# Kernel optimization log

Measured on AMD Instinct MI355X. Metric: run time of the kernel, lower is better.

The kernel has to match this reference:

```python
import jax, jax.numpy as jnp
import numpy as np


def setup_inputs() -> dict:
    key = jax.random.key(0)
    ks = jax.random.split(key, 5)
    B, T, C = 2, 2048, 1024
    x = jax.random.normal(ks[0], (B, T, C), dtype=jnp.float32)
    Wqkv = jax.random.normal(ks[1], (C, 3 * C), dtype=jnp.float32) * (C ** -0.5)
    bqkv = jax.random.normal(ks[2], (3 * C,), dtype=jnp.float32) * 0.02
    Wproj = jax.random.normal(ks[3], (C, C), dtype=jnp.float32) * (C ** -0.5)
    bproj = jax.random.normal(ks[4], (C,), dtype=jnp.float32) * 0.02
    return {"x": x, "Wqkv": Wqkv, "bqkv": bqkv, "Wproj": Wproj, "bproj": bproj}


def reference(x, Wqkv, bqkv, Wproj, bproj):
    B, T, C = x.shape
    n_head = 16
    hd = C // n_head
    x_proj = x @ Wqkv + bqkv  # [B, T, 3C]
    # NOTE: source reshapes (B, T, C) -> (B, n_head, T, hd) directly (no transpose);
    # we replicate that exactly for faithfulness.
    q = x_proj[:, :, :C].reshape(B, n_head, T, hd)
    k = x_proj[:, :, C:2 * C].reshape(B, n_head, T, hd)
    v = x_proj[:, :, 2 * C:].reshape(B, n_head, T, hd)
    att = jnp.einsum('bhtd,bhsd->bhts', q, k) * (1.0 / jnp.sqrt(jnp.float32(hd)))
    causal = jnp.tril(jnp.ones((T, T), dtype=bool))  # True where allowed
    att = jnp.where(causal, att, jnp.float32(-jnp.inf))
    att = jax.nn.softmax(att, axis=-1)
    y = att @ v  # [B, H, T, hd]
    y = jnp.transpose(y, (0, 2, 1, 3)).reshape(B, T, C)
    return y @ Wproj + bproj
```

## Files before the change

### kernel.cpp

```cpp
#include <hip/hip_runtime.h>
#include <hip/hip_bf16.h>
#include <stdint.h>

typedef __hip_bfloat16 bf16;
typedef __attribute__((ext_vector_type(8))) short bf16x8;
typedef __attribute__((ext_vector_type(4))) float f32x4;

__device__ __forceinline__ bf16x8 ldsv8(const bf16* p) { return *(const bf16x8*)p; }

__device__ __forceinline__ short bf_bits(float f) {
  union { bf16 h; short s; } u; u.h = __float2bfloat16(f); return u.s;
}

#define ASYNC16(ldsdst, gsrc)                                                  \
  __builtin_amdgcn_global_load_lds(                                            \
      (const __attribute__((address_space(1))) void*)(gsrc),                   \
      (__attribute__((address_space(3))) void*)(ldsdst), 16, 0, 0)

__device__ __forceinline__ bool is_bf16(const void* p) {
  const uint32_t* w = (const uint32_t*)p;
  int cnt = 0;
#pragma unroll 8
  for (int i = 0; i < 64; ++i) {
    uint32_t e = (w[i] >> 7) & 0xffu;
    cnt += (e >= 100u && e <= 150u) ? 1 : 0;
  }
  return cnt >= 40;
}

__device__ __forceinline__ float load_f32(const void* p, size_t idx, bool b16) {
  return b16 ? __bfloat162float(((const bf16*)p)[idx]) : ((const float*)p)[idx];
}

__device__ __forceinline__ void cvtT_body(const void* in, bf16* out, int R,
                                          int Ccols, int bx, int by,
                                          bf16 (*tile)[33]) {
  const bool b16 = is_bf16(in);
  int tx = threadIdx.x & 31, ty = threadIdx.x >> 5;
  int c0 = bx * 32, r0 = by * 32;
#pragma unroll
  for (int i = 0; i < 32; i += 8)
    tile[ty + i][tx] = __float2bfloat16(load_f32(in, (size_t)(r0 + ty + i) * Ccols + c0 + tx, b16));
  __syncthreads();
#pragma unroll
  for (int i = 0; i < 32; i += 8)
    out[(size_t)(c0 + ty + i) * R + r0 + tx] = tile[tx][ty + i];
}

__global__ __launch_bounds__(256) void prep_k(const float* __restrict__ x,
                                              bf16* __restrict__ xb,
                                              const void* __restrict__ Wqkv,
                                              bf16* __restrict__ WqkvT,
                                              const void* __restrict__ Wproj,
                                              bf16* __restrict__ WprojT) {
  __shared__ __align__(16) bf16 tile[32][33];
  const int id = blockIdx.x;
  if (id < 2048) {
    size_t i = (size_t)id * 256 + threadIdx.x;
    const float4 f0 = ((const float4*)x)[i * 2];
    const float4 f1 = ((const float4*)x)[i * 2 + 1];
    bf16x8 pk = {bf_bits(f0.x), bf_bits(f0.y), bf_bits(f0.z), bf_bits(f0.w),
                 bf_bits(f1.x), bf_bits(f1.y), bf_bits(f1.z), bf_bits(f1.w)};
    ((bf16x8*)xb)[i] = pk;
  } else if (id < 5120) {
    int id2 = id - 2048;
    cvtT_body(Wqkv, WqkvT, 1024, 3072, id2 % 96, id2 / 96, tile);
  } else {
    int id3 = id - 5120;
    cvtT_body(Wproj, WprojT, 1024, 1024, id3 % 32, id3 / 32, tile);
  }
}

__global__ __launch_bounds__(256) void cvtT_k(const void* __restrict__ in,
                                              bf16* __restrict__ out,
                                              int R, int Ccols) {
  __shared__ __align__(16) bf16 tile[32][33];
  cvtT_body(in, out, R, Ccols, blockIdx.x, blockIdx.y, tile);
}

__global__ __launch_bounds__(256) void cvt_k(const float* __restrict__ in,
                                             bf16* __restrict__ out) {
  size_t i = (size_t)blockIdx.x * 256 + threadIdx.x;
  const float4 f0 = ((const float4*)in)[i * 2];
  const float4 f1 = ((const float4*)in)[i * 2 + 1];
  bf16x8 pk = {bf_bits(f0.x), bf_bits(f0.y), bf_bits(f0.z), bf_bits(f0.w),
               bf_bits(f1.x), bf_bits(f1.y), bf_bits(f1.z), bf_bits(f1.w)};
  ((bf16x8*)out)[i] = pk;
}

template <int MODE, int BN>
__global__ __launch_bounds__(256) void gemm128(
    const void* __restrict__ Araw, const bf16* __restrict__ BT,
    const void* __restrict__ biasraw, void* __restrict__ outv) {
  constexpr int K = 1024;
  constexpr int NBF = BN / 32;
  __shared__ __align__(16) bf16 As[128 * 32];
  __shared__ __align__(16) bf16 Bs[BN * 32];
  const int tid = threadIdx.x;
  const int wave = tid >> 6, lane = tid & 63;
  const int quad = lane >> 4, l16 = lane & 15;
  const int nwg = gridDim.x * gridDim.y;
  const int lin = blockIdx.y * gridDim.x + blockIdx.x;
  const int swz = (lin & 7) * (nwg >> 3) + (lin >> 3);
  const int m0 = (swz % gridDim.x) * 128, n0 = (swz / gridDim.x) * BN;
  const int wm = (wave & 1) * 64, wn = (wave >> 1) * (BN / 2);
  const bool a16 = (MODE == 0) ? is_bf16(Araw) : true;
  const bool bias16 = is_bf16(biasraw);

  f32x4 acc[4][NBF] = {};

  for (int kt = 0; kt < K; kt += 32) {
    __syncthreads();
    if (MODE != 0 || a16) {
#pragma unroll
      for (int i = 0; i < 2; ++i) {
        int slot = i * 256 + tid;
        int row = slot >> 2, col = (slot & 3) << 3;
        ASYNC16(As + slot * 8, ((const bf16*)Araw) + (size_t)(m0 + row) * K + kt + col);
      }
#pragma unroll
      for (int i = 0; i < BN / 64; ++i) {
        int slot = i * 256 + tid;
        int row = slot >> 2, col = (slot & 3) << 3;
        ASYNC16(Bs + slot * 8, BT + (size_t)(n0 + row) * K + kt + col);
      }
    } else {
#pragma unroll
      for (int i = 0; i < 2; ++i) {
        int slot = i * 256 + tid;
        int row = slot >> 2, col = (slot & 3) << 3;
        const float* ap = ((const float*)Araw) + (size_t)(m0 + row) * K + kt + col;
        float4 f0 = *(const float4*)ap;
        float4 f1 = *(const float4*)(ap + 4);
        bf16x8 pk = {bf_bits(f0.x), bf_bits(f0.y), bf_bits(f0.z), bf_bits(f0.w),
                     bf_bits(f1.x), bf_bits(f1.y), bf_bits(f1.z), bf_bits(f1.w)};
        *(bf16x8*)(As + slot * 8) = pk;
        if (i * 256 < BN * 4)
          *(bf16x8*)(Bs + slot * 8) = *(const bf16x8*)(BT + (size_t)(n0 + row) * K + kt + col);
      }
    }
    __syncthreads();
    bf16x8 af[4], bfr[NBF];
#pragma unroll
    for (int i = 0; i < 4; ++i)
      af[i] = ldsv8(As + (wm + i * 16 + l16) * 32 + quad * 8);
#pragma unroll
    for (int j = 0; j < NBF; ++j)
      bfr[j] = ldsv8(Bs + (wn + j * 16 + l16) * 32 + quad * 8);
#pragma unroll
    for (int i = 0; i < 4; ++i)
#pragma unroll
      for (int j = 0; j < NBF; ++j)
        acc[i][j] = __builtin_amdgcn_mfma_f32_16x16x32_bf16(af[i], bfr[j], acc[i][j], 0, 0, 0);
  }

  float biasf[NBF];
#pragma unroll
  for (int j = 0; j < NBF; ++j)
    biasf[j] = load_f32(biasraw, n0 + wn + j * 16 + l16, bias16);

#pragma unroll
  for (int i = 0; i < 4; ++i)
#pragma unroll
    for (int j = 0; j < NBF; ++j) {
      int ng = n0 + wn + j * 16 + l16;
#pragma unroll
      for (int r = 0; r < 4; ++r) {
        int mg = m0 + wm + i * 16 + quad * 4 + r;
        float v = acc[i][j][r] + biasf[j];
        if (MODE == 1) {
          ((float*)outv)[(size_t)mg * 1024 + ng] = v;
        } else {
          ((bf16*)outv)[(size_t)mg * 3072 + ng] =
              __float2bfloat16(ng < 1024 ? v * 0.125f : v);
        }
      }
    }
}

__global__ __launch_bounds__(512) void attn_k(const bf16* __restrict__ xproj,
                                              bf16* __restrict__ Yb) {
  __shared__ __align__(16) bf16 Ks[128 * 72];
  __shared__ __align__(16) bf16 VTs[64 * 136];
  __shared__ __align__(16) bf16 Ps[8 * 16 * 136];

  const int tid = threadIdx.x;
  const int wave = tid >> 6, lane = tid & 63;
  const int quad = lane >> 4, l16 = lane & 15;
  const int pid = blockIdx.x;
  const int qtA = pid, qtB = 15 - pid;
  const int bh = blockIdx.y, b = bh >> 4, h = bh & 15;
  const size_t rowbase = (size_t)(b * 2048 + h * 128) * 3072;
  const int q0[2] = {qtA * 128, qtB * 128};

  bf16x8 aq[2][2];
#pragma unroll
  for (int t = 0; t < 2; ++t) {
    int sg = q0[t] + wave * 16 + l16;
    const bf16* qp = xproj + rowbase + (size_t)(sg >> 4) * 3072 + ((sg & 15) << 6);
#pragma unroll
    for (int ks = 0; ks < 2; ++ks)
      aq[t][ks] = *(const bf16x8*)(qp + ks * 32 + quad * 8);
  }

  f32x4 o[2][4] = {};
  float mrow[2][4], lrow[2][4];
#pragma unroll
  for (int t = 0; t < 2; ++t)
#pragma unroll
    for (int r = 0; r < 4; ++r) { mrow[t][r] = -1e30f; lrow[t][r] = 0.f; }

  bf16* Pw = Ps + wave * (16 * 136);

  const int slot0 = tid, slot1 = 512 + tid;
  const int sA = slot0 >> 3, blkA = slot0 & 7;
  const int sB = slot1 >> 3, blkB = slot1 & 7;

  bf16x8 kreg[2], vreg[2];
#define ISSUE_LOADS(stv)                                                        \
  {                                                                             \
    int sg0 = (stv)*128 + sA, sg1 = (stv)*128 + sB;                             \
    const bf16* b0 = xproj + rowbase + (size_t)(sg0 >> 4) * 3072 + ((sg0 & 15) << 6); \
    const bf16* b1 = xproj + rowbase + (size_t)(sg1 >> 4) * 3072 + ((sg1 & 15) << 6); \
    kreg[0] = *(const bf16x8*)(b0 + 1024 + blkA * 8);                           \
    vreg[0] = *(const bf16x8*)(b0 + 2048 + blkA * 8);                           \
    kreg[1] = *(const bf16x8*)(b1 + 1024 + blkB * 8);                           \
    vreg[1] = *(const bf16x8*)(b1 + 2048 + blkB * 8);                           \
  }

  ISSUE_LOADS(0);

  for (int st = 0; st <= qtB; ++st) {
    __syncthreads();
    {
      *(bf16x8*)(Ks + sA * 72 + blkA * 8) = kreg[0];
      const bf16* ve0 = (const bf16*)&vreg[0];
      const int ssw0 = sA ^ (blkA << 3);
#pragma unroll
      for (int j = 0; j < 8; ++j) VTs[(blkA * 8 + j) * 136 + ssw0] = ve0[j];
      *(bf16x8*)(Ks + sB * 72 + blkB * 8) = kreg[1];
      const bf16* ve1 = (const bf16*)&vreg[1];
      const int ssw1 = sB ^ (blkB << 3);
#pragma unroll
      for (int j = 0; j < 8; ++j) VTs[(blkB * 8 + j) * 136 + ssw1] = ve1[j];
    }
    if (st < qtB) ISSUE_LOADS(st + 1);
    __syncthreads();

    const bool doA = (st <= qtA);
#pragma unroll
    for (int t = 0; t < 2; ++t) {
      if (t == 0 && !doA) continue;
      const bool diag = (st == (t == 0 ? qtA : qtB));

      f32x4 sc[8] = {};
      __builtin_amdgcn_s_setprio(1);
#pragma unroll
      for (int ks = 0; ks < 2; ++ks)
#pragma unroll
        for (int j = 0; j < 8; ++j) {
          bf16x8 bk = ldsv8(Ks + (j * 16 + l16) * 72 + (ks * 4 + quad) * 8);
          sc[j] = __builtin_amdgcn_mfma_f32_16x16x32_bf16(aq[t][ks], bk, sc[j], 0, 0, 0);
        }
      __builtin_amdgcn_s_setprio(0);

#pragma unroll
      for (int r = 0; r < 4; ++r) {
        const int rloc = wave * 16 + quad * 4 + r;
        float vals[8];
        float mx = -1e30f;
#pragma unroll
        for (int j = 0; j < 8; ++j) {
          float v = sc[j][r];
          if (diag && (j * 16 + l16) > rloc) v = -1e30f;
          vals[j] = v;
          mx = fmaxf(mx, v);
        }
#pragma unroll
        for (int d = 1; d < 16; d <<= 1) mx = fmaxf(mx, __shfl_xor(mx, d, 64));
        float mnew = fmaxf(mrow[t][r], mx);
        float alpha = __expf(mrow[t][r] - mnew);
        mrow[t][r] = mnew;
        float rs = 0.f;
#pragma unroll
        for (int j = 0; j < 8; ++j) {
          float p = __expf(vals[j] - mnew);
          vals[j] = p;
          rs += p;
        }
#pragma unroll
        for (int d = 1; d < 16; d <<= 1) rs += __shfl_xor(rs, d, 64);
        lrow[t][r] = lrow[t][r] * alpha + rs;
#pragma unroll
        for (int j = 0; j < 4; ++j) o[t][j][r] *= alpha;
        bf16* prow = Pw + (quad * 4 + r) * 136;
        const int psw = quad << 3;
#pragma unroll
        for (int j = 0; j < 8; ++j) prow[(j * 16 + l16) ^ psw] = __float2bfloat16(vals[j]);
      }

      __builtin_amdgcn_s_setprio(1);
#pragma unroll
      for (int ks = 0; ks < 4; ++ks) {
        bf16x8 ap = ldsv8(Pw + l16 * 136 + (((ks * 4 + quad) ^ (l16 >> 2)) << 3));
#pragma unroll
        for (int j = 0; j < 4; ++j) {
          int d = j * 16 + l16;
          bf16x8 bv = ldsv8(VTs + d * 136 + (((ks * 4 + quad) ^ (2 * j + (l16 >> 3))) << 3));
          o[t][j] = __builtin_amdgcn_mfma_f32_16x16x32_bf16(ap, bv, o[t][j], 0, 0, 0);
        }
      }
      __builtin_amdgcn_s_setprio(0);
    }
  }
#undef ISSUE_LOADS

  bf16* Yh = Yb + (size_t)b * 2097152 + h * 64;
#pragma unroll
  for (int t = 0; t < 2; ++t)
#pragma unroll
    for (int r = 0; r < 4; ++r) {
      int tt = q0[t] + wave * 16 + quad * 4 + r;
      float inv = 1.f / lrow[t][r];
#pragma unroll
      for (int j = 0; j < 4; ++j)
        Yh[(size_t)tt * 1024 + j * 16 + l16] = __float2bfloat16(o[t][j][r] * inv);
    }
}

extern "C" void kernel_launch(void* const* d_in, const int* in_sizes, int n_in,
                              void* d_out, int out_size, void* d_ws, size_t ws_size,
                              hipStream_t stream) {
  (void)out_size;
  const void* px     = d_in[0];
  const void* pWqkv  = (n_in > 1) ? d_in[1] : d_in[0];
  const void* pbqkv  = (n_in > 2) ? d_in[2] : d_in[0];
  const void* pWproj = (n_in > 3) ? d_in[3] : d_in[0];
  const void* pbproj = (n_in > 4) ? d_in[4] : d_in[0];
  for (int i = 0; i < n_in; ++i) {
    switch (in_sizes[i]) {
      case 4194304: px     = d_in[i]; break;
      case 3145728: pWqkv  = d_in[i]; break;
      case 3072:    pbqkv  = d_in[i]; break;
      case 1048576: pWproj = d_in[i]; break;
      case 1024:    pbproj = d_in[i]; break;
      default: break;
    }
  }

  char* ws = (char*)d_ws;
  bf16* xproj = (bf16*)(ws + 0);

  if (ws_size >= 41943040) {
    bf16* xb     = (bf16*)(ws + 25165824);
    bf16* WqkvT  = (bf16*)(ws + 33554432);
    bf16* WprojT = (bf16*)(ws + 39845888);
    bf16* Yb     = (bf16*)(ws + 27262976);

    prep_k<<<dim3(6144), 256, 0, stream>>>((const float*)px, xb, pWqkv, WqkvT,
                                           pWproj, WprojT);
    gemm128<0, 128><<<dim3(32, 24), 256, 0, stream>>>(xb, WqkvT, pbqkv, xproj);
    attn_k<<<dim3(8, 32), 512, 0, stream>>>(xproj, Yb);
    gemm128<1, 64><<<dim3(32, 16), 256, 0, stream>>>(Yb, WprojT, pbproj, d_out);
  } else if (ws_size >= 39845888) {
    bf16* xb     = (bf16*)(ws + 25165824);
    bf16* WqkvT  = (bf16*)(ws + 33554432);
    bf16* WprojT = (bf16*)(ws + 25165824);
    bf16* Yb     = (bf16*)(ws + 27262976);

    cvt_k<<<dim3(2048), 256, 0, stream>>>((const float*)px, xb);
    cvtT_k<<<dim3(96, 32), 256, 0, stream>>>(pWqkv, WqkvT, 1024, 3072);
    gemm128<0, 128><<<dim3(32, 24), 256, 0, stream>>>(xb, WqkvT, pbqkv, xproj);
    cvtT_k<<<dim3(32, 32), 256, 0, stream>>>(pWproj, WprojT, 1024, 1024);
    attn_k<<<dim3(8, 32), 512, 0, stream>>>(xproj, Yb);
    gemm128<1, 64><<<dim3(32, 16), 256, 0, stream>>>(Yb, WprojT, pbproj, d_out);
  } else {
    bf16* WqkvT  = (bf16*)(ws + 25165824);
    bf16* WprojT = (bf16*)(ws + 25165824);
    bf16* Yb     = (bf16*)(ws + 27262976);

    cvtT_k<<<dim3(96, 32), 256, 0, stream>>>(pWqkv, WqkvT, 1024, 3072);
    gemm128<0, 128><<<dim3(32, 24), 256, 0, stream>>>(px, WqkvT, pbqkv, xproj);
    cvtT_k<<<dim3(32, 32), 256, 0, stream>>>(pWproj, WprojT, 1024, 1024);
    attn_k<<<dim3(8, 32), 512, 0, stream>>>(xproj, Yb);
    gemm128<1, 64><<<dim3(32, 16), 256, 0, stream>>>(Yb, WprojT, pbproj, d_out);
  }
}
```

Before: 207.1 us.

## Double-buffer K/V shared-memory tiles in attention to drop one barrier per step

Makes the K and transposed-V LDS tiles double-buffered and prefetches two tiles ahead in registers, so each step writes the next tile into the alternate buffer after computing and needs a single __syncthreads instead of two. The aim is to cut barrier stalls and let global loads overlap more compute. In exchange it roughly doubles K/V LDS use, which may lower occupancy at 512 threads per block.

```diff
diff --git a/kernel.cpp b/kernel.cpp
--- a/kernel.cpp
+++ b/kernel.cpp
@@ -180,8 +180,10 @@
 
 __global__ __launch_bounds__(512) void attn_k(const bf16* __restrict__ xproj,
                                               bf16* __restrict__ Yb) {
-  __shared__ __align__(16) bf16 Ks[128 * 72];
-  __shared__ __align__(16) bf16 VTs[64 * 136];
+  constexpr int KSZ = 128 * 72;
+  constexpr int VSZ = 64 * 136;
+  __shared__ __align__(16) bf16 Ks[2 * KSZ];
+  __shared__ __align__(16) bf16 VTs[2 * VSZ];
   __shared__ __align__(16) bf16 Ps[8 * 16 * 136];
 
   const int tid = threadIdx.x;
@@ -227,25 +229,31 @@
     kreg[1] = *(const bf16x8*)(b1 + 1024 + blkB * 8);                           \
     vreg[1] = *(const bf16x8*)(b1 + 2048 + blkB * 8);                           \
   }
+#define WRITE_TILE(buf)                                                         \
+  {                                                                             \
+    bf16* Kd = Ks + (buf)*KSZ;                                                  \
+    bf16* Vd = VTs + (buf)*VSZ;                                                 \
+    *(bf16x8*)(Kd + sA * 72 + blkA * 8) = kreg[0];                              \
+    const bf16* ve0 = (const bf16*)&vreg[0];                                    \
+    const int ssw0 = sA ^ (blkA << 3);                                          \
+    _Pragma("unroll")                                                           \
+    for (int j = 0; j < 8; ++j) Vd[(blkA * 8 + j) * 136 + ssw0] = ve0[j];       \
+    *(bf16x8*)(Kd + sB * 72 + blkB * 8) = kreg[1];                              \
+    const bf16* ve1 = (const bf16*)&vreg[1];                                    \
+    const int ssw1 = sB ^ (blkB << 3);                                          \
+    _Pragma("unroll")                                                           \
+    for (int j = 0; j < 8; ++j) Vd[(blkB * 8 + j) * 136 + ssw1] = ve1[j];       \
+  }
 
   ISSUE_LOADS(0);
-
+  WRITE_TILE(0);
+  ISSUE_LOADS(1);
+  __syncthreads();
+
+  int cur = 0;
   for (int st = 0; st <= qtB; ++st) {
-    __syncthreads();
-    {
-      *(bf16x8*)(Ks + sA * 72 + blkA * 8) = kreg[0];
-      const bf16* ve0 = (const bf16*)&vreg[0];
-      const int ssw0 = sA ^ (blkA << 3);
-#pragma unroll
-      for (int j = 0; j < 8; ++j) VTs[(blkA * 8 + j) * 136 + ssw0] = ve0[j];
-      *(bf16x8*)(Ks + sB * 72 + blkB * 8) = kreg[1];
-      const bf16* ve1 = (const bf16*)&vreg[1];
-      const int ssw1 = sB ^ (blkB << 3);
-#pragma unroll
-      for (int j = 0; j < 8; ++j) VTs[(blkB * 8 + j) * 136 + ssw1] = ve1[j];
-    }
-    if (st < qtB) ISSUE_LOADS(st + 1);
-    __syncthreads();
+    const bf16* Kc = Ks + cur * KSZ;
+    const bf16* Vc = VTs + cur * VSZ;
 
     const bool doA = (st <= qtA);
 #pragma unroll
@@ -259,7 +267,7 @@
       for (int ks = 0; ks < 2; ++ks)
 #pragma unroll
         for (int j = 0; j < 8; ++j) {
-          bf16x8 bk = ldsv8(Ks + (j * 16 + l16) * 72 + (ks * 4 + quad) * 8);
+          bf16x8 bk = ldsv8(Kc + (j * 16 + l16) * 72 + (ks * 4 + quad) * 8);
           sc[j] = __builtin_amdgcn_mfma_f32_16x16x32_bf16(aq[t][ks], bk, sc[j], 0, 0, 0);
         }
       __builtin_amdgcn_s_setprio(0);
@@ -306,14 +314,22 @@
 #pragma unroll
         for (int j = 0; j < 4; ++j) {
           int d = j * 16 + l16;
-          bf16x8 bv = ldsv8(VTs + d * 136 + (((ks * 4 + quad) ^ (2 * j + (l16 >> 3))) << 3));
+          bf16x8 bv = ldsv8(Vc + d * 136 + (((ks * 4 + quad) ^ (2 * j + (l16 >> 3))) << 3));
           o[t][j] = __builtin_amdgcn_mfma_f32_16x16x32_bf16(ap, bv, o[t][j], 0, 0, 0);
         }
       }
       __builtin_amdgcn_s_setprio(0);
     }
+
+    if (st < qtB) {
+      WRITE_TILE(cur ^ 1);
+      if (st + 2 <= qtB) ISSUE_LOADS(st + 2);
+      __syncthreads();
+      cur ^= 1;
+    }
   }
 #undef ISSUE_LOADS
+#undef WRITE_TILE
 
   bf16* Yh = Yb + (size_t)b * 2097152 + h * 64;
 #pragma unroll
```

New measurement: 207.4 us. No clear change (+0.2%).
